# Kernel optimization log

Measured on AMD Instinct MI355X. Metric: run time of the kernel, lower is better.

## Reference

```python
import jax, jax.numpy as jnp
import numpy as np

B, NV, NQ, NA = 128, 100, 14, 10
V_DIM, Q_DIM, A_DIM = 2048, 1024, 1024
H_DIM, RANK, HD, G = 512, 32, 16, 2  # HD = H_DIM // RANK, G = glimpse


def setup_inputs() -> dict:
    key = jax.random.key(0)
    ks = jax.random.split(key, 16)
    s = 0.05
    return {
        "v": jax.random.normal(ks[0], (B, NV, V_DIM), jnp.float32),
        "q": jax.random.normal(ks[1], (B, NQ, Q_DIM), jnp.float32),
        "a": jax.random.normal(ks[2], (B, NA, A_DIM), jnp.float32),
        # tucker projections (FCNet = Linear + ReLU; dropout identity at eval)
        "Wv": jax.random.normal(ks[3], (H_DIM, V_DIM), jnp.float32) * s,
        "bv": jnp.zeros((H_DIM,), jnp.float32),
        "Wq": jax.random.normal(ks[4], (H_DIM, Q_DIM), jnp.float32) * s,
        "bq": jnp.zeros((H_DIM,), jnp.float32),
        "Wa": jax.random.normal(ks[5], (H_DIM, A_DIM), jnp.float32) * s,
        "ba": jnp.zeros((H_DIM,), jnp.float32),
        # rank-wise projection nets, stacked over rank: [rank, HD, H_DIM]
        "Wvr": jax.random.normal(ks[6], (RANK, HD, H_DIM), jnp.float32) * s,
        "bvr": jnp.zeros((RANK, HD), jnp.float32),
        "Wqr": jax.random.normal(ks[7], (RANK, HD, H_DIM), jnp.float32) * s,
        "bqr": jnp.zeros((RANK, HD), jnp.float32),
        "War": jax.random.normal(ks[8], (RANK, HD, H_DIM), jnp.float32) * s,
        "bar": jnp.zeros((RANK, HD), jnp.float32),
        # Tucker core T_g with h_out squeezed: [rank, hv, hq, ha, glimpse]
        "T": jax.random.normal(ks[9], (RANK, HD, HD, HD, G), jnp.float32),
    }


def reference(v, q, a, Wv, bv, Wq, bq, Wa, ba, Wvr, bvr, Wqr, bqr, War, bar, T):
    relu = jax.nn.relu
    # modality tucker projections: [B, N, H_DIM]
    vt = relu(jnp.einsum('bnd,hd->bnh', v, Wv) + bv)
    qt = relu(jnp.einsum('bnd,hd->bnh', q, Wq) + bq)
    at = relu(jnp.einsum('bnd,hd->bnh', a, Wa) + ba)
    # rank-wise FCNets, batched over rank: [B, rank, N, HD]
    v_ = relu(jnp.einsum('bnh,rch->brnc', vt, Wvr) + bvr[None, :, None, :])
    q_ = relu(jnp.einsum('bnh,rch->brnc', qt, Wqr) + bqr[None, :, None, :])
    a_ = relu(jnp.einsum('bnh,rch->brnc', at, War) + bar[None, :, None, :])
    # 6-way Tucker contraction, summed over rank: [B, NV, NQ, NA, G]
    f_emb = jnp.einsum('rijkg,bnvi,bnqj,bnak->bvqag', T, v_, q_, a_,
                       optimize=True)
    return f_emb
```

## Files before the change

kernel.cpp:

```cpp
#include <hip/hip_runtime.h>
#include <cstddef>
#include <cstdint>

#define B_    128
#define NV_   100
#define NQ_   14
#define NA_   10
#define HDIM  512
#define RANK_ 32
#define HD_   16
#define G_    2

typedef __bf16 bf16x8 __attribute__((ext_vector_type(8)));
typedef float  f32x4  __attribute__((ext_vector_type(4)));
union Frag { uint4 u; bf16x8 v; };

__device__ __forceinline__ unsigned int f2bf(float f) {
  unsigned int u = __float_as_uint(f);
  u = (u + 0x7FFFu + ((u >> 16) & 1u)) >> 16;
  return u & 0xFFFFu;
}

__global__ __launch_bounds__(256) void cvt_kernel(
    const float* __restrict__ s0, const float* __restrict__ s1,
    const float* __restrict__ s2, const float* __restrict__ s3,
    const float* __restrict__ s4, const float* __restrict__ s5,
    const float* __restrict__ s6, const float* __restrict__ s7,
    unsigned short* __restrict__ dst)
{
  const int pref[8] = {896, 1536, 2048, 2304, 2560, 2688, 2816, 2944};
  const float* srcs[8] = {s0, s1, s2, s3, s4, s5, s6, s7};
  const int blk = blockIdx.x;
  int seg = 0;
  #pragma unroll
  for (int i = 0; i < 7; ++i) if (blk >= pref[i]) seg = i + 1;
  const int base_chunk = seg ? pref[seg - 1] : 0;
  const size_t loc = (size_t)(blk - base_chunk) * 2048 + threadIdx.x * 8;
  const float* s = srcs[seg] + loc;
  float4 f0 = *(const float4*)s;
  float4 f1 = *(const float4*)(s + 4);
  ushort4 o0, o1;
  o0.x = f2bf(f0.x); o0.y = f2bf(f0.y); o0.z = f2bf(f0.z); o0.w = f2bf(f0.w);
  o1.x = f2bf(f1.x); o1.y = f2bf(f1.y); o1.z = f2bf(f1.z); o1.w = f2bf(f1.w);
  unsigned short* d = dst + (size_t)blk * 2048 + threadIdx.x * 8;
  *(ushort4*)d = o0;
  *(ushort4*)(d + 4) = o1;
}

__device__ __forceinline__ void stage_swz(const unsigned short* __restrict__ src,
                                          int K, unsigned short* dst, int t)
{
  const int w64 = t & 192;
  const int l = t & 63;
  #pragma unroll
  for (int i = 0; i < 4; ++i) {
    const int sb = i * 256 + w64;
    const int li = sb + l;
    const int row = li >> 3;
    const int p = li & 7;
    const int s = p ^ (row & 7);
    const unsigned short* gp = src + (size_t)row * K + s * 8;
    unsigned short* dp = dst + sb * 8;
    __builtin_amdgcn_global_load_lds(
        (const __attribute__((address_space(1))) void*)gp,
        (__attribute__((address_space(3))) void*)dp, 16, 0, 0);
  }
}

__global__ __launch_bounds__(256, 2) void l1_gemm(
    const float* __restrict__ v,
    const unsigned short* __restrict__ qb, const unsigned short* __restrict__ ab,
    const unsigned short* __restrict__ Wvb, const unsigned short* __restrict__ Wqb,
    const unsigned short* __restrict__ Wab,
    const float* __restrict__ bv, const float* __restrict__ bq,
    const float* __restrict__ ba,
    unsigned short* __restrict__ vtb, unsigned short* __restrict__ qtb,
    unsigned short* __restrict__ atb)
{
  __shared__ __align__(16) unsigned short As[2][8192];
  __shared__ __align__(16) unsigned short Bs[2][8192];
  const int bx = blockIdx.x;
  int grp, gx, gy, K;
  const unsigned short *A16 = qb, *W;
  const float* bias;
  unsigned short* C;
  if (bx < 400) {
    grp = 0; const int xcd = bx & 7, j = bx >> 3; const int m = xcd * 50 + j;
    gy = m >> 2; gx = m & 3; W = Wvb; bias = bv; C = vtb; K = 2048;
  } else if (bx < 456) {
    grp = 1; const int lo = bx - 400; gy = lo >> 2; gx = lo & 3;
    A16 = qb; W = Wqb; bias = bq; C = qtb; K = 1024;
  } else {
    grp = 2; const int lo = bx - 456; gy = lo >> 2; gx = lo & 3;
    A16 = ab; W = Wab; bias = ba; C = atb; K = 1024;
  }
  const int nsteps = K >> 6;
  const int bm = gy * 128, bn = gx * 128;
  const int t = threadIdx.x;
  const int w = t >> 6, l = t & 63;
  const int wm = (w >> 1) * 64, wn = (w & 1) * 64;

  f32x4 acc[4][4];
  #pragma unroll
  for (int i = 0; i < 4; ++i)
    #pragma unroll
    for (int j = 0; j < 4; ++j) acc[i][j] = f32x4{0.f, 0.f, 0.f, 0.f};

  const int ar = t >> 1, kh = t & 1;
  const float* vrow = (grp == 0)
      ? v + (size_t)(bm + ar) * 2048 + kh * 32 : (const float*)nullptr;

  stage_swz(W + (size_t)bn * K, K, Bs[0], t);
  if (grp == 0) {
    float4 f[8];
    #pragma unroll
    for (int i = 0; i < 8; ++i) f[i] = ((const float4*)vrow)[i];
    unsigned short* abp = &As[0][ar * 64];
    #pragma unroll
    for (int s2 = 0; s2 < 4; ++s2) {
      uint4 p;
      p.x = f2bf(f[2*s2].x)   | (f2bf(f[2*s2].y)   << 16);
      p.y = f2bf(f[2*s2].z)   | (f2bf(f[2*s2].w)   << 16);
      p.z = f2bf(f[2*s2+1].x) | (f2bf(f[2*s2+1].y) << 16);
      p.w = f2bf(f[2*s2+1].z) | (f2bf(f[2*s2+1].w) << 16);
      const int sx = (kh * 4 + s2) ^ (ar & 7);
      *(uint4*)&abp[sx * 8] = p;
    }
  } else {
    stage_swz(A16 + (size_t)bm * K, K, As[0], t);
  }
  __syncthreads();

  for (int step = 0; step < nsteps; ++step) {
    const int db = step & 1;
    const bool hn = (step + 1) < nsteps;
    const int k0n = (step + 1) << 6;
    float4 f[8];
    if (hn) {
      stage_swz(W + (size_t)bn * K + k0n, K, Bs[db ^ 1], t);
      if (grp == 0) {
        #pragma unroll
        for (int i = 0; i < 8; ++i) f[i] = ((const float4*)(vrow + k0n))[i];
      } else {
        stage_swz(A16 + (size_t)bm * K + k0n, K, As[db ^ 1], t);
      }
    }
    const unsigned short* Ad = As[db];
    const unsigned short* Bd = Bs[db];
    #pragma unroll
    for (int ks = 0; ks < 2; ++ks) {
      Frag fa[4], fb[4];
      #pragma unroll
      for (int i = 0; i < 4; ++i) {
        const int r = wm + 16 * i + (l & 15);
        fa[i].u = *(const uint4*)&Ad[r * 64 + (((ks * 4 + (l >> 4)) ^ (r & 7)) * 8)];
      }
      #pragma unroll
      for (int j = 0; j < 4; ++j) {
        const int r = wn + 16 * j + (l & 15);
        fb[j].u = *(const uint4*)&Bd[r * 64 + (((ks * 4 + (l >> 4)) ^ (r & 7)) * 8)];
      }
      #pragma unroll
      for (int i = 0; i < 4; ++i)
        #pragma unroll
        for (int j = 0; j < 4; ++j)
          acc[i][j] = __builtin_amdgcn_mfma_f32_16x16x32_bf16(fa[i].v, fb[j].v, acc[i][j], 0, 0, 0);
    }
    if (hn && grp == 0) {
      unsigned short* abp = &As[db ^ 1][ar * 64];
      #pragma unroll
      for (int s2 = 0; s2 < 4; ++s2) {
        uint4 p;
        p.x = f2bf(f[2*s2].x)   | (f2bf(f[2*s2].y)   << 16);
        p.y = f2bf(f[2*s2].z)   | (f2bf(f[2*s2].w)   << 16);
        p.z = f2bf(f[2*s2+1].x) | (f2bf(f[2*s2+1].y) << 16);
        p.w = f2bf(f[2*s2+1].z) | (f2bf(f[2*s2+1].w) << 16);
        const int sx = (kh * 4 + s2) ^ (ar & 7);
        *(uint4*)&abp[sx * 8] = p;
      }
    }
    __syncthreads();
  }

  const int q4 = (l >> 4) * 4, cl = l & 15;
  #pragma unroll
  for (int i = 0; i < 4; ++i)
    #pragma unroll
    for (int j = 0; j < 4; ++j) {
      const int col = bn + wn + 16 * j + cl;
      const float bs = bias[col];
      #pragma unroll
      for (int r = 0; r < 4; ++r) {
        const int row = bm + wm + 16 * i + q4 + r;
        float o = fmaxf(acc[i][j][r] + bs, 0.f);
        C[(size_t)row * 512 + col] = (unsigned short)f2bf(o);
      }
    }
}

__global__ __launch_bounds__(256, 2) void l2_gemm(
    const unsigned short* __restrict__ vtb, const unsigned short* __restrict__ qtb,
    const unsigned short* __restrict__ atb,
    const unsigned short* __restrict__ Wvrb, const unsigned short* __restrict__ Wqrb,
    const unsigned short* __restrict__ Warb,
    const float* __restrict__ bvr, const float* __restrict__ bqr,
    const float* __restrict__ bar,
    unsigned short* __restrict__ vrb, float* __restrict__ q_r, float* __restrict__ a_r)
{
  __shared__ __align__(16) unsigned short As[2][8192];
  __shared__ __align__(16) unsigned short Bs[2][8192];
  const int bx = blockIdx.x;
  int grp, gx, gy;
  const unsigned short *A16, *W;
  const float* bias;
  if (bx < 400) {
    grp = 0; const int xcd = bx & 7, j = bx >> 3; const int m = xcd * 50 + j;
    gy = m >> 2; gx = m & 3; A16 = vtb; W = Wvrb; bias = bvr;
  } else if (bx < 456) {
    grp = 1; const int lo = bx - 400; gy = lo >> 2; gx = lo & 3;
    A16 = qtb; W = Wqrb; bias = bqr;
  } else {
    grp = 2; const int lo = bx - 456; gy = lo >> 2; gx = lo & 3;
    A16 = atb; W = Warb; bias = bar;
  }
  const int bm = gy * 128, bn = gx * 128;
  const int t = threadIdx.x;
  const int w = t >> 6, l = t & 63;
  const int wm = (w >> 1) * 64, wn = (w & 1) * 64;

  f32x4 acc[4][4];
  #pragma unroll
  for (int i = 0; i < 4; ++i)
    #pragma unroll
    for (int j = 0; j < 4; ++j) acc[i][j] = f32x4{0.f, 0.f, 0.f, 0.f};

  stage_swz(W + (size_t)bn * 512, 512, Bs[0], t);
  stage_swz(A16 + (size_t)bm * 512, 512, As[0], t);
  __syncthreads();

  for (int step = 0; step < 8; ++step) {
    const int db = step & 1;
    const bool hn = (step + 1) < 8;
    const int k0n = (step + 1) << 6;
    if (hn) {
      stage_swz(W + (size_t)bn * 512 + k0n, 512, Bs[db ^ 1], t);
      stage_swz(A16 + (size_t)bm * 512 + k0n, 512, As[db ^ 1], t);
    }
    const unsigned short* Ad = As[db];
    const unsigned short* Bd = Bs[db];
    #pragma unroll
    for (int ks = 0; ks < 2; ++ks) {
      Frag fa[4], fb[4];
      #pragma unroll
      for (int i = 0; i < 4; ++i) {
        const int r = wm + 16 * i + (l & 15);
        fa[i].u = *(const uint4*)&Ad[r * 64 + (((ks * 4 + (l >> 4)) ^ (r & 7)) * 8)];
      }
      #pragma unroll
      for (int j = 0; j < 4; ++j) {
        const int r = wn + 16 * j + (l & 15);
        fb[j].u = *(const uint4*)&Bd[r * 64 + (((ks * 4 + (l >> 4)) ^ (r & 7)) * 8)];
      }
      #pragma unroll
      for (int i = 0; i < 4; ++i)
        #pragma unroll
        for (int j = 0; j < 4; ++j)
          acc[i][j] = __builtin_amdgcn_mfma_f32_16x16x32_bf16(fa[i].v, fb[j].v, acc[i][j], 0, 0, 0);
    }
    __syncthreads();
  }

  const int q4 = (l >> 4) * 4, cl = l & 15;
  #pragma unroll
  for (int i = 0; i < 4; ++i)
    #pragma unroll
    for (int j = 0; j < 4; ++j) {
      const int col = bn + wn + 16 * j + cl;
      const float bs = bias[col];
      #pragma unroll
      for (int r = 0; r < 4; ++r) {
        const int row = bm + wm + 16 * i + q4 + r;
        float o = fmaxf(acc[i][j][r] + bs, 0.f);
        if (grp == 0)      vrb[(size_t)row * 512 + col] = (unsigned short)f2bf(o);
        else if (grp == 1) q_r[(size_t)row * 512 + col] = o;
        else               a_r[(size_t)row * 512 + col] = o;
      }
    }
}

__global__ void tsum_kernel(const float* __restrict__ T, float* __restrict__ Tsum)
{
  const int idx = blockIdx.x * 256 + threadIdx.x;
  float s = 0.f;
  #pragma unroll
  for (int r = 0; r < RANK_; ++r) s += T[r * 8192 + idx];
  Tsum[idx] = s;
}

__global__ __launch_bounds__(256) void build_w_kernel(
    const float* __restrict__ q_, const float* __restrict__ a_,
    const float* __restrict__ Tsum, unsigned short* __restrict__ WmatT)
{
  const int n = blockIdx.x, b = blockIdx.y, t = threadIdx.x;
  __shared__ float Ts[8192];
  __shared__ float U[14 * 544];

  #pragma unroll
  for (int s = 0; s < 8; ++s)
    ((float4*)Ts)[s * 256 + t] = ((const float4*)Tsum)[s * 256 + t];
  __syncthreads();

  {
    const int i = t >> 4, k = t & 15;
    float acc0[NQ_], acc1[NQ_];
    #pragma unroll
    for (int q = 0; q < NQ_; ++q) { acc0[q] = 0.f; acc1[q] = 0.f; }
    const float* qbase = q_ + (size_t)b * NQ_ * HDIM + n * 16;
    #pragma unroll
    for (int j = 0; j < 16; ++j) {
      float2 ts = *(const float2*)&Ts[i * 512 + j * 32 + k * 2];
      #pragma unroll
      for (int q = 0; q < NQ_; ++q) {
        float qv = qbase[q * HDIM + j];
        acc0[q] += ts.x * qv;
        acc1[q] += ts.y * qv;
      }
    }
    #pragma unroll
    for (int q = 0; q < NQ_; ++q) {
      float2 uu; uu.x = acc0[q]; uu.y = acc1[q];
      *(float2*)&U[q * 544 + i * 34 + k * 2] = uu;
    }
  }
  __syncthreads();

  if ((t >> 4) < NQ_) {
    const int q = t >> 4, i = t & 15;
    float acc0[NA_], acc1[NA_];
    #pragma unroll
    for (int a = 0; a < NA_; ++a) { acc0[a] = 0.f; acc1[a] = 0.f; }
    const float* abase = a_ + (size_t)b * NA_ * HDIM + n * 16;
    #pragma unroll
    for (int k = 0; k < 16; ++k) {
      float2 uu = *(const float2*)&U[q * 544 + i * 34 + k * 2];
      #pragma unroll
      for (int a = 0; a < NA_; ++a) {
        float av = abase[a * HDIM + k];
        acc0[a] += uu.x * av;
        acc1[a] += uu.y * av;
      }
    }
    unsigned short* wb = WmatT + (size_t)b * 320 * 512 + (n * 16 + i);
    #pragma unroll
    for (int a = 0; a < NA_; ++a) {
      wb[(size_t)((q * 10 + a) * 2 + 0) * 512] = (unsigned short)f2bf(acc0[a]);
      wb[(size_t)((q * 10 + a) * 2 + 1) * 512] = (unsigned short)f2bf(acc1[a]);
    }
  }
}

__global__ __launch_bounds__(256) void final_mfma(
    const unsigned short* __restrict__ Vrb, const unsigned short* __restrict__ WmatT,
    float* __restrict__ out)
{
  __shared__ __align__(16) unsigned short As[2048];
  __shared__ __align__(16) unsigned short Bs[5120];
  const int b  = blockIdx.y;
  const int mh = blockIdx.x >> 1;
  const int n0 = (blockIdx.x & 1) * 160;
  const int t = threadIdx.x;
  const int w = t >> 6, l = t & 63;
  const int wm = (w >> 1) * 32;
  const int wn = (w & 1) * 80;

  f32x4 acc[2][5];
  #pragma unroll
  for (int mi = 0; mi < 2; ++mi)
    #pragma unroll
    for (int nj = 0; nj < 5; ++nj) acc[mi][nj] = f32x4{0.f, 0.f, 0.f, 0.f};

  const unsigned short* Wb = WmatT + (size_t)b * 320 * 512;

  for (int k0 = 0; k0 < 512; k0 += 32) {
    {
      int grow = b * NV_ + mh * 64 + w * 16 + (l >> 2);
      if (grow > B_ * NV_ - 1) grow = B_ * NV_ - 1;
      const unsigned short* src = Vrb + (size_t)grow * HDIM + k0 + (l & 3) * 8;
      __builtin_amdgcn_global_load_lds(
          (const __attribute__((address_space(1))) void*)src,
          (__attribute__((address_space(3))) void*)&As[w * 512], 16, 0, 0);
    }
    #pragma unroll
    for (int c = 0; c < 3; ++c) {
      const int base = c * 256 + w * 64;
      if (base < 640) {
        const int li = base + l;
        const int nrow = li >> 2, ko2 = (li & 3) * 8;
        const unsigned short* src = Wb + (size_t)(n0 + nrow) * 512 + k0 + ko2;
        __builtin_amdgcn_global_load_lds(
            (const __attribute__((address_space(1))) void*)src,
            (__attribute__((address_space(3))) void*)&Bs[base * 8], 16, 0, 0);
      }
    }
    __syncthreads();

    Frag fa[2], fb[5];
    #pragma unroll
    for (int mi = 0; mi < 2; ++mi)
      fa[mi].u = *(const uint4*)&As[(wm + mi * 16 + (l & 15)) * 32 + (l >> 4) * 8];
    #pragma unroll
    for (int nj = 0; nj < 5; ++nj)
      fb[nj].u = *(const uint4*)&Bs[(wn + nj * 16 + (l & 15)) * 32 + (l >> 4) * 8];
    #pragma unroll
    for (int mi = 0; mi < 2; ++mi)
      #pragma unroll
      for (int nj = 0; nj < 5; ++nj)
        acc[mi][nj] = __builtin_amdgcn_mfma_f32_16x16x32_bf16(fa[mi].v, fb[nj].v, acc[mi][nj], 0, 0, 0);
    __syncthreads();
  }

  #pragma unroll
  for (int mi = 0; mi < 2; ++mi)
    #pragma unroll
    for (int nj = 0; nj < 5; ++nj) {
      const int col = n0 + wn + nj * 16 + (l & 15);
      if (col < 280) {
        #pragma unroll
        for (int r = 0; r < 4; ++r) {
          const int row = mh * 64 + wm + mi * 16 + (l >> 4) * 4 + r;
          if (row < NV_)
            out[((size_t)b * NV_ + row) * 280 + col] = acc[mi][nj][r];
        }
      }
    }
}

extern "C" void kernel_launch(void* const* d_in, const int* in_sizes, int n_in,
                              void* d_out, int out_size, void* d_ws, size_t ws_size,
                              hipStream_t stream)
{
  const float* v   = (const float*)d_in[0];
  const float* q   = (const float*)d_in[1];
  const float* a   = (const float*)d_in[2];
  const float* Wv  = (const float*)d_in[3];
  const float* bv  = (const float*)d_in[4];
  const float* Wq  = (const float*)d_in[5];
  const float* bq  = (const float*)d_in[6];
  const float* Wa  = (const float*)d_in[7];
  const float* ba  = (const float*)d_in[8];
  const float* Wvr = (const float*)d_in[9];
  const float* bvr = (const float*)d_in[10];
  const float* Wqr = (const float*)d_in[11];
  const float* bqr = (const float*)d_in[12];
  const float* War = (const float*)d_in[13];
  const float* bar = (const float*)d_in[14];
  const float* T   = (const float*)d_in[15];

  unsigned short* wsu = (unsigned short*)d_ws;
  float* wsf = (float*)d_ws;

  unsigned short* WmatT = wsu;
  unsigned short* qb    = wsu;
  unsigned short* ab    = wsu + 1835008;
  unsigned short* Wvb   = wsu + 3145728;
  unsigned short* Wqb   = wsu + 4194304;
  unsigned short* Wab   = wsu + 4718592;
  unsigned short* Wvrb  = wsu + 5242880;
  unsigned short* Wqrb  = wsu + 5505024;
  unsigned short* Warb  = wsu + 5767168;
  unsigned short* vtb   = wsu + 20971520;
  unsigned short* qtb   = wsu + 27525120;
  unsigned short* atb   = wsu + 28442624;
  unsigned short* vrb   = wsu + 29097984;
  float* q_r  = wsf + 17825792;
  float* a_r  = wsf + 18743296;
  float* Tsum = wsf + 19398656;

  cvt_kernel<<<2944, 256, 0, stream>>>(q, a, Wv, Wq, Wa, Wvr, Wqr, War, wsu);

  l1_gemm<<<496, 256, 0, stream>>>(v, qb, ab, Wvb, Wqb, Wab, bv, bq, ba,
                                   vtb, qtb, atb);
  l2_gemm<<<496, 256, 0, stream>>>(vtb, qtb, atb, Wvrb, Wqrb, Warb,
                                   bvr, bqr, bar, vrb, q_r, a_r);

  tsum_kernel<<<32, 256, 0, stream>>>(T, Tsum);
  build_w_kernel<<<dim3(32, 128), 256, 0, stream>>>(q_r, a_r, Tsum, WmatT);
  final_mfma<<<dim3(4, 128), 256, 0, stream>>>(vrb, WmatT, (float*)d_out);
}
```

Before: 347.5 us.

## Use 512-thread GEMM blocks, prefetch v two steps ahead, double-buffer final MFMA

The l1 and l2 GEMMs move from 256 to 512 threads per block, giving 8 waves that each compute a 64x32 sub-tile, with staging split across more threads. l1 keeps two register buffers of fp32 v rows so global loads run two k-steps ahead of the bf16 convert-and-write into LDS. final_mfma gets double-buffered LDS so the next k-slice loads while the current one feeds the MFMAs, and it drops one barrier per step. The goal is to hide memory latency and raise occupancy, at the cost of more LDS, more registers and smaller per-wave tiles with less fragment reuse.

```diff
diff --git a/kernel.cpp b/kernel.cpp
--- a/kernel.cpp
+++ b/kernel.cpp
@@ -19,6 +19,13 @@
   unsigned int u = __float_as_uint(f);
   u = (u + 0x7FFFu + ((u >> 16) & 1u)) >> 16;
   return u & 0xFFFFu;
+}
+
+__device__ __forceinline__ void gload_lds16(const unsigned short* gp,
+                                            unsigned short* dp) {
+  __builtin_amdgcn_global_load_lds(
+      (const __attribute__((address_space(1))) void*)gp,
+      (__attribute__((address_space(3))) void*)dp, 16, 0, 0);
 }
 
 __global__ __launch_bounds__(256) void cvt_kernel(
@@ -47,27 +54,39 @@
   *(ushort4*)(d + 4) = o1;
 }
 
-__device__ __forceinline__ void stage_swz(const unsigned short* __restrict__ src,
-                                          int K, unsigned short* dst, int t)
-{
-  const int w64 = t & 192;
+__device__ __forceinline__ void stage_swz8(const unsigned short* __restrict__ src,
+                                           int K, unsigned short* dst, int t)
+{
+  const int wb = t & 448;
   const int l = t & 63;
   #pragma unroll
-  for (int i = 0; i < 4; ++i) {
-    const int sb = i * 256 + w64;
+  for (int i = 0; i < 2; ++i) {
+    const int sb = i * 512 + wb;
     const int li = sb + l;
     const int row = li >> 3;
     const int p = li & 7;
     const int s = p ^ (row & 7);
-    const unsigned short* gp = src + (size_t)row * K + s * 8;
-    unsigned short* dp = dst + sb * 8;
-    __builtin_amdgcn_global_load_lds(
-        (const __attribute__((address_space(1))) void*)gp,
-        (__attribute__((address_space(3))) void*)dp, 16, 0, 0);
-  }
-}
-
-__global__ __launch_bounds__(256, 2) void l1_gemm(
+    gload_lds16(src + (size_t)row * K + s * 8, dst + sb * 8);
+  }
+}
+
+__device__ __forceinline__ void cvt_write(const float4 f[4], unsigned short* Abuf,
+                                          int ar, int kq)
+{
+  unsigned short* base = Abuf + ar * 64;
+  #pragma unroll
+  for (int j = 0; j < 2; ++j) {
+    uint4 p;
+    p.x = f2bf(f[2*j].x)   | (f2bf(f[2*j].y)   << 16);
+    p.y = f2bf(f[2*j].z)   | (f2bf(f[2*j].w)   << 16);
+    p.z = f2bf(f[2*j+1].x) | (f2bf(f[2*j+1].y) << 16);
+    p.w = f2bf(f[2*j+1].z) | (f2bf(f[2*j+1].w) << 16);
+    const int s = (kq * 2 + j) ^ (ar & 7);
+    *(uint4*)&base[s * 8] = p;
+  }
+}
+
+__global__ __launch_bounds__(512, 4) void l1_gemm(
     const float* __restrict__ v,
     const unsigned short* __restrict__ qb, const unsigned short* __restrict__ ab,
     const unsigned short* __restrict__ Wvb, const unsigned short* __restrict__ Wqb,
@@ -98,87 +117,74 @@
   const int bm = gy * 128, bn = gx * 128;
   const int t = threadIdx.x;
   const int w = t >> 6, l = t & 63;
-  const int wm = (w >> 1) * 64, wn = (w & 1) * 64;
-
-  f32x4 acc[4][4];
+  const int wm = (w >> 2) * 64, wn = (w & 3) * 32;
+
+  f32x4 acc[4][2];
   #pragma unroll
   for (int i = 0; i < 4; ++i)
     #pragma unroll
-    for (int j = 0; j < 4; ++j) acc[i][j] = f32x4{0.f, 0.f, 0.f, 0.f};
-
-  const int ar = t >> 1, kh = t & 1;
+    for (int j = 0; j < 2; ++j) acc[i][j] = f32x4{0.f, 0.f, 0.f, 0.f};
+
+  const int ar = t >> 2, kq = t & 3;
   const float* vrow = (grp == 0)
-      ? v + (size_t)(bm + ar) * 2048 + kh * 32 : (const float*)nullptr;
-
-  stage_swz(W + (size_t)bn * K, K, Bs[0], t);
+      ? v + (size_t)(bm + ar) * 2048 + kq * 16 : (const float*)nullptr;
+  float4 R0[4], R1[4];
+
+  stage_swz8(W + (size_t)bn * K, K, Bs[0], t);
   if (grp == 0) {
-    float4 f[8];
-    #pragma unroll
-    for (int i = 0; i < 8; ++i) f[i] = ((const float4*)vrow)[i];
-    unsigned short* abp = &As[0][ar * 64];
-    #pragma unroll
-    for (int s2 = 0; s2 < 4; ++s2) {
-      uint4 p;
-      p.x = f2bf(f[2*s2].x)   | (f2bf(f[2*s2].y)   << 16);
-      p.y = f2bf(f[2*s2].z)   | (f2bf(f[2*s2].w)   << 16);
-      p.z = f2bf(f[2*s2+1].x) | (f2bf(f[2*s2+1].y) << 16);
-      p.w = f2bf(f[2*s2+1].z) | (f2bf(f[2*s2+1].w) << 16);
-      const int sx = (kh * 4 + s2) ^ (ar & 7);
-      *(uint4*)&abp[sx * 8] = p;
-    }
+    #pragma unroll
+    for (int i = 0; i < 4; ++i) R0[i] = ((const float4*)vrow)[i];
+    #pragma unroll
+    for (int i = 0; i < 4; ++i) R1[i] = ((const float4*)(vrow + 64))[i];
+    cvt_write(R0, As[0], ar, kq);
   } else {
-    stage_swz(A16 + (size_t)bm * K, K, As[0], t);
+    stage_swz8(A16 + (size_t)bm * K, K, As[0], t);
   }
   __syncthreads();
 
   for (int step = 0; step < nsteps; ++step) {
     const int db = step & 1;
     const bool hn = (step + 1) < nsteps;
-    const int k0n = (step + 1) << 6;
-    float4 f[8];
-    if (hn) {
-      stage_swz(W + (size_t)bn * K + k0n, K, Bs[db ^ 1], t);
-      if (grp == 0) {
-        #pragma unroll
-        for (int i = 0; i < 8; ++i) f[i] = ((const float4*)(vrow + k0n))[i];
-      } else {
-        stage_swz(A16 + (size_t)bm * K + k0n, K, As[db ^ 1], t);
-      }
+    if (hn) stage_swz8(W + (size_t)bn * K + (step + 1) * 64, K, Bs[db ^ 1], t);
+    if (grp == 0) {
+      if (step + 2 < nsteps) {
+        const float* p = vrow + (step + 2) * 64;
+        if (db == 0) {
+          #pragma unroll
+          for (int i = 0; i < 4; ++i) R0[i] = ((const float4*)p)[i];
+        } else {
+          #pragma unroll
+          for (int i = 0; i < 4; ++i) R1[i] = ((const float4*)p)[i];
+        }
+      }
+      if (hn) {
+        if (db == 0) cvt_write(R1, As[1], ar, kq);
+        else         cvt_write(R0, As[0], ar, kq);
+      }
+    } else if (hn) {
+      stage_swz8(A16 + (size_t)bm * K + (step + 1) * 64, K, As[db ^ 1], t);
     }
     const unsigned short* Ad = As[db];
     const unsigned short* Bd = Bs[db];
     #pragma unroll
     for (int ks = 0; ks < 2; ++ks) {
-      Frag fa[4], fb[4];
+      Frag fa[4], fb[2];
       #pragma unroll
       for (int i = 0; i < 4; ++i) {
         const int r = wm + 16 * i + (l & 15);
         fa[i].u = *(const uint4*)&Ad[r * 64 + (((ks * 4 + (l >> 4)) ^ (r & 7)) * 8)];
       }
       #pragma unroll
-      for (int j = 0; j < 4; ++j) {
+      for (int j = 0; j < 2; ++j) {
         const int r = wn + 16 * j + (l & 15);
         fb[j].u = *(const uint4*)&Bd[r * 64 + (((ks * 4 + (l >> 4)) ^ (r & 7)) * 8)];
       }
       #pragma unroll
       for (int i = 0; i < 4; ++i)
         #pragma unroll
-        for (int j = 0; j < 4; ++j)
+        for (int j = 0; j < 2; ++j)
           acc[i][j] = __builtin_amdgcn_mfma_f32_16x16x32_bf16(fa[i].v, fb[j].v, acc[i][j], 0, 0, 0);
     }
-    if (hn && grp == 0) {
-      unsigned short* abp = &As[db ^ 1][ar * 64];
-      #pragma unroll
-      for (int s2 = 0; s2 < 4; ++s2) {
-        uint4 p;
-        p.x = f2bf(f[2*s2].x)   | (f2bf(f[2*s2].y)   << 16);
-        p.y = f2bf(f[2*s2].z)   | (f2bf(f[2*s2].w)   << 16);
-        p.z = f2bf(f[2*s2+1].x) | (f2bf(f[2*s2+1].y) << 16);
-        p.w = f2bf(f[2*s2+1].z) | (f2bf(f[2*s2+1].w) << 16);
-        const int sx = (kh * 4 + s2) ^ (ar & 7);
-        *(uint4*)&abp[sx * 8] = p;
-      }
-    }
     __syncthreads();
   }
 
@@ -186,7 +192,7 @@
   #pragma unroll
   for (int i = 0; i < 4; ++i)
     #pragma unroll
-    for (int j = 0; j < 4; ++j) {
+    for (int j = 0; j < 2; ++j) {
       const int col = bn + wn + 16 * j + cl;
       const float bs = bias[col];
       #pragma unroll
@@ -198,7 +204,7 @@
     }
 }
 
-__global__ __launch_bounds__(256, 2) void l2_gemm(
+__global__ __launch_bounds__(512, 4) void l2_gemm(
     const unsigned short* __restrict__ vtb, const unsigned short* __restrict__ qtb,
     const unsigned short* __restrict__ atb,
     const unsigned short* __restrict__ Wvrb, const unsigned short* __restrict__ Wqrb,
@@ -226,16 +232,16 @@
   const int bm = gy * 128, bn = gx * 128;
   const int t = threadIdx.x;
   const int w = t >> 6, l = t & 63;
-  const int wm = (w >> 1) * 64, wn = (w & 1) * 64;
-
-  f32x4 acc[4][4];
+  const int wm = (w >> 2) * 64, wn = (w & 3) * 32;
+
+  f32x4 acc[4][2];
   #pragma unroll
   for (int i = 0; i < 4; ++i)
     #pragma unroll
-    for (int j = 0; j < 4; ++j) acc[i][j] = f32x4{0.f, 0.f, 0.f, 0.f};
-
-  stage_swz(W + (size_t)bn * 512, 512, Bs[0], t);
-  stage_swz(A16 + (size_t)bm * 512, 512, As[0], t);
+    for (int j = 0; j < 2; ++j) acc[i][j] = f32x4{0.f, 0.f, 0.f, 0.f};
+
+  stage_swz8(W + (size_t)bn * 512, 512, Bs[0], t);
+  stage_swz8(A16 + (size_t)bm * 512, 512, As[0], t);
   __syncthreads();
 
   for (int step = 0; step < 8; ++step) {
@@ -243,28 +249,28 @@
     const bool hn = (step + 1) < 8;
     const int k0n = (step + 1) << 6;
     if (hn) {
-      stage_swz(W + (size_t)bn * 512 + k0n, 512, Bs[db ^ 1], t);
-      stage_swz(A16 + (size_t)bm * 512 + k0n, 512, As[db ^ 1], t);
+      stage_swz8(W + (size_t)bn * 512 + k0n, 512, Bs[db ^ 1], t);
+      stage_swz8(A16 + (size_t)bm * 512 + k0n, 512, As[db ^ 1], t);
     }
     const unsigned short* Ad = As[db];
     const unsigned short* Bd = Bs[db];
     #pragma unroll
     for (int ks = 0; ks < 2; ++ks) {
-      Frag fa[4], fb[4];
+      Frag fa[4], fb[2];
       #pragma unroll
       for (int i = 0; i < 4; ++i) {
         const int r = wm + 16 * i + (l & 15);
         fa[i].u = *(const uint4*)&Ad[r * 64 + (((ks * 4 + (l >> 4)) ^ (r & 7)) * 8)];
       }
       #pragma unroll
-      for (int j = 0; j < 4; ++j) {
+      for (int j = 0; j < 2; ++j) {
         const int r = wn + 16 * j + (l & 15);
         fb[j].u = *(const uint4*)&Bd[r * 64 + (((ks * 4 + (l >> 4)) ^ (r & 7)) * 8)];
       }
       #pragma unroll
       for (int i = 0; i < 4; ++i)
         #pragma unroll
-        for (int j = 0; j < 4; ++j)
+        for (int j = 0; j < 2; ++j)
           acc[i][j] = __builtin_amdgcn_mfma_f32_16x16x32_bf16(fa[i].v, fb[j].v, acc[i][j], 0, 0, 0);
     }
     __syncthreads();
@@ -274,7 +280,7 @@
   #pragma unroll
   for (int i = 0; i < 4; ++i)
     #pragma unroll
-    for (int j = 0; j < 4; ++j) {
+    for (int j = 0; j < 2; ++j) {
       const int col = bn + wn + 16 * j + cl;
       const float bs = bias[col];
       #pragma unroll
@@ -359,12 +365,34 @@
   }
 }
 
+__device__ __forceinline__ void final_stage(
+    const unsigned short* __restrict__ Vrb, const unsigned short* __restrict__ Wb,
+    int b, int mh, int n0, int k0, int t,
+    unsigned short* Asb, unsigned short* Bsb)
+{
+  const int w = t >> 6, l = t & 63;
+  {
+    int grow = b * NV_ + mh * 64 + w * 16 + (l >> 2);
+    if (grow > B_ * NV_ - 1) grow = B_ * NV_ - 1;
+    gload_lds16(Vrb + (size_t)grow * HDIM + k0 + (l & 3) * 8, &Asb[w * 512]);
+  }
+  #pragma unroll
+  for (int c = 0; c < 3; ++c) {
+    const int base = c * 256 + w * 64;
+    if (base < 640) {
+      const int li = base + l;
+      const int nrow = li >> 2, ko2 = (li & 3) * 8;
+      gload_lds16(Wb + (size_t)(n0 + nrow) * 512 + k0 + ko2, &Bsb[base * 8]);
+    }
+  }
+}
+
 __global__ __launch_bounds__(256) void final_mfma(
     const unsigned short* __restrict__ Vrb, const unsigned short* __restrict__ WmatT,
     float* __restrict__ out)
 {
-  __shared__ __align__(16) unsigned short As[2048];
-  __shared__ __align__(16) unsigned short Bs[5120];
+  __shared__ __align__(16) unsigned short As[2][2048];
+  __shared__ __align__(16) unsigned short Bs[2][5120];
   const int b  = blockIdx.y;
   const int mh = blockIdx.x >> 1;
   const int n0 = (blockIdx.x & 1) * 160;
@@ -381,36 +409,21 @@
 
   const unsigned short* Wb = WmatT + (size_t)b * 320 * 512;
 
-  for (int k0 = 0; k0 < 512; k0 += 32) {
-    {
-      int grow = b * NV_ + mh * 64 + w * 16 + (l >> 2);
-      if (grow > B_ * NV_ - 1) grow = B_ * NV_ - 1;
-      const unsigned short* src = Vrb + (size_t)grow * HDIM + k0 + (l & 3) * 8;
-      __builtin_amdgcn_global_load_lds(
-          (const __attribute__((address_space(1))) void*)src,
-          (__attribute__((address_space(3))) void*)&As[w * 512], 16, 0, 0);
-    }
-    #pragma unroll
-    for (int c = 0; c < 3; ++c) {
-      const int base = c * 256 + w * 64;
-      if (base < 640) {
-        const int li = base + l;
-        const int nrow = li >> 2, ko2 = (li & 3) * 8;
-        const unsigned short* src = Wb + (size_t)(n0 + nrow) * 512 + k0 + ko2;
-        __builtin_amdgcn_global_load_lds(
-            (const __attribute__((address_space(1))) void*)src,
-            (__attribute__((address_space(3))) void*)&Bs[base * 8], 16, 0, 0);
-      }
-    }
-    __syncthreads();
+  final_stage(Vrb, Wb, b, mh, n0, 0, t, As[0], Bs[0]);
+  __syncthreads();
+
+  for (int step = 0; step < 16; ++step) {
+    const int db = step & 1;
+    if (step + 1 < 16)
+      final_stage(Vrb, Wb, b, mh, n0, (step + 1) * 32, t, As[db ^ 1], Bs[db ^ 1]);
 
     Frag fa[2], fb[5];
     #pragma unroll
     for (int mi = 0; mi < 2; ++mi)
-      fa[mi].u = *(const uint4*)&As[(wm + mi * 16 + (l & 15)) * 32 + (l >> 4) * 8];
+      fa[mi].u = *(const uint4*)&As[db][(wm + mi * 16 + (l & 15)) * 32 + (l >> 4) * 8];
     #pragma unroll
     for (int nj = 0; nj < 5; ++nj)
-      fb[nj].u = *(const uint4*)&Bs[(wn + nj * 16 + (l & 15)) * 32 + (l >> 4) * 8];
+      fb[nj].u = *(const uint4*)&Bs[db][(wn + nj * 16 + (l & 15)) * 32 + (l >> 4) * 8];
     #pragma unroll
     for (int mi = 0; mi < 2; ++mi)
       #pragma unroll
@@ -478,9 +491,9 @@
 
   cvt_kernel<<<2944, 256, 0, stream>>>(q, a, Wv, Wq, Wa, Wvr, Wqr, War, wsu);
 
-  l1_gemm<<<496, 256, 0, stream>>>(v, qb, ab, Wvb, Wqb, Wab, bv, bq, ba,
+  l1_gemm<<<496, 512, 0, stream>>>(v, qb, ab, Wvb, Wqb, Wab, bv, bq, ba,
                                    vtb, qtb, atb);
-  l2_gemm<<<496, 256, 0, stream>>>(vtb, qtb, atb, Wvrb, Wqrb, Warb,
+  l2_gemm<<<496, 512, 0, stream>>>(vtb, qtb, atb, Wvrb, Wqrb, Warb,
                                    bvr, bqr, bar, vrb, q_r, a_r);
 
   tsum_kernel<<<32, 256, 0, stream>>>(T, Tsum);
```

New measurement: 328.0 us. -5.6%, faster.
